# Kernel optimization log

Measured on AMD Instinct MI355X. Metric: run time of the kernel, lower is better.

## Reference

```python
import jax, jax.numpy as jnp
import numpy as np

B, L, D = 2, 2048, 1024
H = 16
HD = D // H  # 64
WINDOW = 256


def setup_inputs() -> dict:
    key = jax.random.key(0)
    k1, k2, k3 = jax.random.split(key, 3)
    s = 0.02
    return {
        "x": jax.random.normal(k1, (B, L, D), dtype=jnp.float32),
        "w_qkv": jax.random.normal(k2, (D, 3 * D), dtype=jnp.float32) * s,
        "b_qkv": jnp.zeros((3 * D,), dtype=jnp.float32),
        "w_out": jax.random.normal(k3, (D, D), dtype=jnp.float32) * s,
        "b_out": jnp.zeros((D,), dtype=jnp.float32),
    }


def _window_mask(seq_len, window_size, dtype):
    # row i allows cols in [i - w//2, i + w//2] inclusive (symmetric band)
    half = window_size // 2
    i = jnp.arange(seq_len)[:, None]
    j = jnp.arange(seq_len)[None, :]
    allowed = jnp.abs(i - j) <= half
    return jnp.where(allowed, jnp.zeros((), dtype), jnp.asarray(-jnp.inf, dtype))


def reference(x, w_qkv, b_qkv, w_out, b_out):
    b, l, d = x.shape
    qkv = x @ w_qkv + b_qkv                        # [B, L, 3D]
    qkv = qkv.reshape(b, l, 3, H, HD)
    q = jnp.transpose(qkv[:, :, 0], (0, 2, 1, 3))   # [B, H, L, HD]
    k = jnp.transpose(qkv[:, :, 1], (0, 2, 1, 3))
    v = jnp.transpose(qkv[:, :, 2], (0, 2, 1, 3))
    scale = 1.0 / np.sqrt(HD)
    scores = jnp.einsum("bhqd,bhkd->bhqk", q, k) * scale
    scores = scores + _window_mask(l, WINDOW, scores.dtype)[None, None]
    attn = jax.nn.softmax(scores, axis=-1)          # dropout: eval mode (p applied only in training)
    out = jnp.einsum("bhqk,bhkd->bhqd", attn, v)    # [B, H, L, HD]
    out = jnp.transpose(out, (0, 2, 1, 3)).reshape(b, l, d)
    return out @ w_out + b_out
```

## Files before the change

kernel.cpp:

```cpp
#include <hip/hip_runtime.h>
#include <math.h>

#define B_    2
#define L_    2048
#define D_    1024
#define H_    16
#define HD_   64
#define HALF_ 128
#define TQ    32
#define PST   296

typedef __attribute__((ext_vector_type(8))) short short8;
typedef __attribute__((ext_vector_type(4))) float f32x4;

__device__ __forceinline__ unsigned short f2bf(float x) {
  unsigned int u = __float_as_uint(x);
  u = (u + 0x7fffu + ((u >> 16) & 1u)) >> 16;
  return (unsigned short)u;
}

__device__ __forceinline__ void async_cp16(const unsigned short* g, unsigned short* l) {
  __builtin_amdgcn_global_load_lds(
      (const __attribute__((address_space(1))) unsigned int*)g,
      (__attribute__((address_space(3))) unsigned int*)l, 16, 0, 0);
}

__device__ __forceinline__ void tr_round32(const float* __restrict__ in,
                                           unsigned short* __restrict__ hi,
                                           int N, int K, int n0, int k0,
                                           float (*t)[33], int tid) {
  {
    const int kl = tid >> 3, nl = (tid & 7) * 4;
    const float4 v = *(const float4*)&in[(size_t)(k0 + kl) * N + n0 + nl];
    t[kl][nl + 0] = v.x; t[kl][nl + 1] = v.y;
    t[kl][nl + 2] = v.z; t[kl][nl + 3] = v.w;
  }
  __syncthreads();
  {
    const int no = tid >> 3, ko = (tid & 7) * 4;
    ushort4 h;
    h.x = f2bf(t[ko + 0][no]);
    h.y = f2bf(t[ko + 1][no]);
    h.z = f2bf(t[ko + 2][no]);
    h.w = f2bf(t[ko + 3][no]);
    *(ushort4*)&hi[(size_t)(n0 + no) * K + k0 + ko] = h;
  }
}

__global__ __launch_bounds__(256) void prep(const float* __restrict__ x,
                                            unsigned short* __restrict__ x_hi,
                                            const float* __restrict__ w_qkv,
                                            unsigned short* __restrict__ wqkvT,
                                            const float* __restrict__ w_out,
                                            unsigned short* __restrict__ woutT) {
  __shared__ float t[32][33];
  const int bx = blockIdx.x, tid = threadIdx.x;
  if (bx < 4096) {
    const int i = (bx * 256 + tid) * 4;
    const float4 a = *(const float4*)&x[i];
    ushort4 h;
    h.x = f2bf(a.x); h.y = f2bf(a.y); h.z = f2bf(a.z); h.w = f2bf(a.w);
    *(ushort4*)&x_hi[i] = h;
  } else if (bx < 7168) {
    const int tb = bx - 4096;
    tr_round32(w_qkv, wqkvT, 3 * D_, D_, (tb % 96) * 32, (tb / 96) * 32, t, tid);
  } else {
    const int tb = bx - 7168;
    tr_round32(w_out, woutT, D_, D_, (tb % 32) * 32, (tb / 32) * 32, t, tid);
  }
}

__global__ __launch_bounds__(256, 3) void gemm_qkv(
    const unsigned short* __restrict__ Ah,
    const unsigned short* __restrict__ Bh,
    const float* __restrict__ bias,
    unsigned short* __restrict__ q_hi,
    unsigned short* __restrict__ kT,
    unsigned short* __restrict__ vTile,
    int N, int K) {
  __shared__ char smraw[33792];
  const int tid  = threadIdx.x;
  const int wave = tid >> 6, lane = tid & 63;

  const int lin = blockIdx.y * gridDim.x + blockIdx.x;
  const int swz = (lin & 7) * 96 + (lin >> 3);
  const int n0 = (swz % 24) * 128, m0 = (swz / 24) * 128;

  const int wm = (wave >> 1) * 64, wn = (wave & 1) * 64;
  const int quad = lane >> 4, ln16 = lane & 15;

  const bool isA = wave < 2;
  const unsigned short* src = isA ? Ah : Bh;
  const int baserow = isA ? m0 : n0;
  const int instbase = (wave & 1) * 8;
  const int dbase = (isA ? 0 : 16384) + instbase * 1024;
  size_t goff[8];
#pragma unroll
  for (int i = 0; i < 8; ++i) {
    const int r = (instbase + i) * 8 + (lane >> 3);
    const int c = (lane & 7) ^ (r & 7);
    goff[i] = (size_t)(baserow + r) * K + c * 8;
  }

  int offA[4], offB[4];
#pragma unroll
  for (int t = 0; t < 4; ++t) {
    const int r = wm + t * 16 + ln16;
    offA[t] = r * 128 + ((quad ^ (r & 7)) * 16);
    const int rn = wn + t * 16 + ln16;
    offB[t] = 16384 + rn * 128 + ((quad ^ (rn & 7)) * 16);
  }

  f32x4 acc[4][4] = {};
  const char* smb = (const char*)smraw;

  for (int k0 = 0; k0 < K; k0 += 64) {
#pragma unroll
    for (int i = 0; i < 8; ++i)
      async_cp16(src + goff[i] + k0,
                 (unsigned short*)(smraw + dbase + i * 1024));
    __syncthreads();

    {
      short8 ah[4], bh[4];
#pragma unroll
      for (int t = 0; t < 4; ++t) {
        ah[t] = *(const short8*)(smb + offA[t]);
        bh[t] = *(const short8*)(smb + offB[t]);
      }
#pragma unroll
      for (int t = 0; t < 4; ++t)
#pragma unroll
        for (int u = 0; u < 4; ++u)
          acc[t][u] = __builtin_amdgcn_mfma_f32_16x16x32_bf16(bh[u], ah[t], acc[t][u], 0, 0, 0);
    }
    {
      short8 ah[4], bh[4];
#pragma unroll
      for (int t = 0; t < 4; ++t) {
        ah[t] = *(const short8*)(smb + (offA[t] ^ 64));
        bh[t] = *(const short8*)(smb + (offB[t] ^ 64));
      }
#pragma unroll
      for (int t = 0; t < 4; ++t)
#pragma unroll
        for (int u = 0; u < 4; ++u)
          acc[t][u] = __builtin_amdgcn_mfma_f32_16x16x32_bf16(bh[u], ah[t], acc[t][u], 0, 0, 0);
    }
    __syncthreads();
  }

  const int slot = n0 >> 10;
  const int nbase = n0 & 1023;

  if (slot == 0) {
#pragma unroll
    for (int t = 0; t < 4; ++t) {
      const int m = m0 + wm + t * 16 + ln16;
#pragma unroll
      for (int u = 0; u < 4; ++u) {
        const int nl = wn + u * 16 + quad * 4;
        const float4 bq = *(const float4*)&bias[n0 + nl];
        ushort4 h;
        h.x = f2bf(acc[t][u][0] + bq.x);
        h.y = f2bf(acc[t][u][1] + bq.y);
        h.z = f2bf(acc[t][u][2] + bq.z);
        h.w = f2bf(acc[t][u][3] + bq.w);
        *(ushort4*)&q_hi[(size_t)m * 1024 + nbase + nl] = h;
      }
    }
  } else if (slot == 1) {
#pragma unroll
    for (int t = 0; t < 4; ++t) {
      const int tok = m0 + wm + t * 16 + ln16;
      const int bb = tok >> 11, j = tok & 2047;
#pragma unroll
      for (int u = 0; u < 4; ++u) {
        const int nl = wn + u * 16 + quad * 4;
        const float4 bq = *(const float4*)&bias[n0 + nl];
        const int hd = nbase + nl;
        const int hh_ = hd >> 6, dg = (hd & 63) >> 3, di = hd & 7;
        ushort4 h;
        h.x = f2bf(acc[t][u][0] + bq.x);
        h.y = f2bf(acc[t][u][1] + bq.y);
        h.z = f2bf(acc[t][u][2] + bq.z);
        h.w = f2bf(acc[t][u][3] + bq.w);
        const size_t o =
            ((((size_t)bb * 16 + hh_) * 8 + dg) * 2048 + j) * 8 + di;
        *(ushort4*)&kT[o] = h;
      }
    }
  } else {
    unsigned short* lt = (unsigned short*)smraw;
#pragma unroll
    for (int t = 0; t < 4; ++t) {
      const int ml = wm + t * 16 + ln16;
#pragma unroll
      for (int u = 0; u < 4; ++u) {
        const int nl = wn + u * 16 + quad * 4;
        const float4 bq = *(const float4*)&bias[n0 + nl];
        ushort4 h;
        h.x = f2bf(acc[t][u][0] + bq.x);
        h.y = f2bf(acc[t][u][1] + bq.y);
        h.z = f2bf(acc[t][u][2] + bq.z);
        h.w = f2bf(acc[t][u][3] + bq.w);
        *(ushort4*)&lt[ml * 132 + nl] = h;
      }
    }
    __syncthreads();
    const int jg0 = (m0 & 2047) >> 3;
    const int bb = m0 >> 11;
#pragma unroll
    for (int it = 0; it < 8; ++it) {
      const int chunk = it * 256 + tid;
      const int hd = chunk & 127, tokg = chunk >> 7;
      short8 hh;
#pragma unroll
      for (int s = 0; s < 8; ++s)
        hh[s] = (short)lt[(tokg * 8 + s) * 132 + hd];
      const size_t o =
          (((size_t)bb * 256 + jg0 + tokg) * 1024 + nbase + hd) * 8;
      *(short8*)&vTile[o] = hh;
    }
  }
}

__global__ __launch_bounds__(256, 2) void gemm_out(
    const unsigned short* __restrict__ Ah,
    const unsigned short* __restrict__ Bh,
    const float* __restrict__ bias,
    float* __restrict__ C,
    int N, int K) {
  __shared__ char smraw[24576];
  const int tid  = threadIdx.x;
  const int wave = tid >> 6, lane = tid & 63;

  const int lin = blockIdx.y * gridDim.x + blockIdx.x;
  const int swz = (lin & 7) * 64 + (lin >> 3);
  const int n0 = (swz % 16) * 64, m0 = (swz / 16) * 128;

  const int quad = lane >> 4, ln16 = lane & 15;
  const int wm = wave * 32;

  const unsigned short* sptr[6];
  int dstoff[6];
#pragma unroll
  for (int s = 0; s < 6; ++s) {
    const int g = wave * 6 + s;
    const bool isA = g < 16;
    const unsigned short* base = isA ? Ah : Bh;
    const int r0 = isA ? g * 8 : (g - 16) * 8;
    const int r = r0 + (lane >> 3);
    const int c = (lane & 7) ^ (r & 7);
    sptr[s] = base + (size_t)((isA ? m0 : n0) + r) * K + c * 8;
    dstoff[s] = isA ? g * 1024 : 16384 + (g - 16) * 1024;
  }

  int offA[2], offB[4];
#pragma unroll
  for (int t = 0; t < 2; ++t) {
    const int r = wm + t * 16 + ln16;
    offA[t] = r * 128 + ((quad ^ (r & 7)) * 16);
  }
#pragma unroll
  for (int u = 0; u < 4; ++u) {
    const int rn = u * 16 + ln16;
    offB[u] = 16384 + rn * 128 + ((quad ^ (rn & 7)) * 16);
  }

  f32x4 acc[2][4] = {};
  const char* smb = (const char*)smraw;

  for (int k0 = 0; k0 < K; k0 += 64) {
#pragma unroll
    for (int s = 0; s < 6; ++s)
      async_cp16(sptr[s] + k0, (unsigned short*)(smraw + dstoff[s]));
    __syncthreads();

    {
      short8 ah[2], bh[4];
#pragma unroll
      for (int t = 0; t < 2; ++t) ah[t] = *(const short8*)(smb + offA[t]);
#pragma unroll
      for (int u = 0; u < 4; ++u) bh[u] = *(const short8*)(smb + offB[u]);
#pragma unroll
      for (int t = 0; t < 2; ++t)
#pragma unroll
        for (int u = 0; u < 4; ++u)
          acc[t][u] = __builtin_amdgcn_mfma_f32_16x16x32_bf16(bh[u], ah[t], acc[t][u], 0, 0, 0);
    }
    {
      short8 ah[2], bh[4];
#pragma unroll
      for (int t = 0; t < 2; ++t) ah[t] = *(const short8*)(smb + (offA[t] ^ 64));
#pragma unroll
      for (int u = 0; u < 4; ++u) bh[u] = *(const short8*)(smb + (offB[u] ^ 64));
#pragma unroll
      for (int t = 0; t < 2; ++t)
#pragma unroll
        for (int u = 0; u < 4; ++u)
          acc[t][u] = __builtin_amdgcn_mfma_f32_16x16x32_bf16(bh[u], ah[t], acc[t][u], 0, 0, 0);
    }
    __syncthreads();
  }

#pragma unroll
  for (int t = 0; t < 2; ++t) {
    const int m = m0 + wm + t * 16 + ln16;
#pragma unroll
    for (int u = 0; u < 4; ++u) {
      const int n = n0 + u * 16 + quad * 4;
      const float4 bq = *(const float4*)&bias[n];
      float4 o;
      o.x = acc[t][u][0] + bq.x;
      o.y = acc[t][u][1] + bq.y;
      o.z = acc[t][u][2] + bq.z;
      o.w = acc[t][u][3] + bq.w;
      *(float4*)&C[(size_t)m * N + n] = o;
    }
  }
}

__global__ __launch_bounds__(256, 4) void attn_mfma(
    const unsigned short* __restrict__ q_hi,
    const unsigned short* __restrict__ kT,
    const unsigned short* __restrict__ vTile,
    unsigned short* __restrict__ attn_h) {
  __shared__ unsigned short P[TQ * PST];
  __shared__ float redS[2][32];

  const int b   = blockIdx.z;
  const int h   = blockIdx.y;
  const int i0  = blockIdx.x * TQ;
  const int tid = threadIdx.x;
  const int wave = tid >> 6, lane = tid & 63;
  const int quad = lane >> 4, ln16 = lane & 15;
  const int mt = wave >> 1, np = wave & 1;
  const int jlo = i0 - HALF_;
  const int rbase = mt * 16 + quad * 4;

  float s[4] = {0.f, 0.f, 0.f, 0.f};
  {
    const size_t qbase =
        (size_t)(b * L_ + i0 + mt * 16 + ln16) * 1024 + h * 64 + quad * 8;
    const short8 qh0 = *(const short8*)&q_hi[qbase];
    const short8 qh1 = *(const short8*)&q_hi[qbase + 32];

    const size_t kb0 = (((size_t)b * 16 + h) * 8 + quad) * 2048 * 8;
    const size_t kb1 = (((size_t)b * 16 + h) * 8 + quad + 4) * 2048 * 8;

#pragma unroll
    for (int c = 0; c < 9; ++c) {
      const int nt   = np + 2 * c;
      const int jabs = jlo + nt * 16 + ln16;
      const int jcl  = min(max(jabs, 0), L_ - 1);
      const short8 kh0 = *(const short8*)&kT[kb0 + (size_t)jcl * 8];
      const short8 kh1 = *(const short8*)&kT[kb1 + (size_t)jcl * 8];

      f32x4 a = {};
      a = __builtin_amdgcn_mfma_f32_16x16x32_bf16(qh0, kh0, a, 0, 0, 0);
      a = __builtin_amdgcn_mfma_f32_16x16x32_bf16(qh1, kh1, a, 0, 0, 0);

      const int colj = nt * 16 + ln16;
#pragma unroll
      for (int e = 0; e < 4; ++e) {
        const int iabs = i0 + rbase + e;
        const bool ok = (jabs >= 0) && (jabs < L_) && (abs(iabs - jabs) <= HALF_);
        const float ev = ok ? __expf(a[e] * 0.125f) : 0.f;
        s[e] += ev;
        P[(rbase + e) * PST + colj] = f2bf(ev);
      }
    }
  }
#pragma unroll
  for (int e = 0; e < 4; ++e) {
    s[e] += __shfl_xor(s[e], 1);
    s[e] += __shfl_xor(s[e], 2);
    s[e] += __shfl_xor(s[e], 4);
    s[e] += __shfl_xor(s[e], 8);
  }
  if (ln16 == 0) {
#pragma unroll
    for (int e = 0; e < 4; ++e) redS[np][rbase + e] = s[e];
  }
  __syncthreads();
  float rinv[4];
#pragma unroll
  for (int e = 0; e < 4; ++e) rinv[e] = 1.f / (s[e] + redS[np ^ 1][rbase + e]);

  f32x4 o[2] = {};
  {
    const int dp = np;
    const char* pb = (const char*)P;
#pragma unroll
    for (int c = 0; c < 9; ++c) {
      const short8 pf =
          *(const short8*)(pb + (mt * 16 + ln16) * (PST * 2) + c * 64 + quad * 16);
      int j0 = jlo + c * 32 + quad * 8;
      j0 = min(max(j0, 0), L_ - 8);
      const size_t jgbase = ((size_t)b * 256 + (j0 >> 3)) * 1024;
#pragma unroll
      for (int t = 0; t < 2; ++t) {
        const size_t vb = (jgbase + (h * 64 + dp * 32 + t * 16 + ln16)) * 8;
        const short8 vh = *(const short8*)&vTile[vb];
        o[t] = __builtin_amdgcn_mfma_f32_16x16x32_bf16(pf, vh, o[t], 0, 0, 0);
      }
    }
  }

  __syncthreads();
  float* ob = (float*)P;
  {
    const int dp = np;
#pragma unroll
    for (int t = 0; t < 2; ++t)
#pragma unroll
      for (int e = 0; e < 4; ++e)
        ob[(rbase + e) * 68 + dp * 32 + t * 16 + ln16] = o[t][e] * rinv[e];
  }
  __syncthreads();
  {
    const int rr = tid >> 3, ck = tid & 7;
    const float* rp = ob + rr * 68 + ck * 8;
    const float4 f0 = *(const float4*)&rp[0];
    const float4 f1 = *(const float4*)&rp[4];
    short8 hh;
    hh[0] = (short)f2bf(f0.x); hh[1] = (short)f2bf(f0.y);
    hh[2] = (short)f2bf(f0.z); hh[3] = (short)f2bf(f0.w);
    hh[4] = (short)f2bf(f1.x); hh[5] = (short)f2bf(f1.y);
    hh[6] = (short)f2bf(f1.z); hh[7] = (short)f2bf(f1.w);
    const size_t oo = ((size_t)(b * L_ + i0 + rr)) * 1024 + h * 64 + ck * 8;
    *(short8*)&attn_h[oo] = hh;
  }
}

extern "C" void kernel_launch(void* const* d_in, const int* in_sizes, int n_in,
                              void* d_out, int out_size, void* d_ws, size_t ws_size,
                              hipStream_t stream) {
  const float* x     = (const float*)d_in[0];
  const float* w_qkv = (const float*)d_in[1];
  const float* b_qkv = (const float*)d_in[2];
  const float* w_out = (const float*)d_in[3];
  const float* b_out = (const float*)d_in[4];
  float* out = (float*)d_out;

  const int M = B_ * L_;

  char* ws = (char*)d_ws;
  unsigned short* x_hi    = (unsigned short*)(ws + 0);
  unsigned short* wqkvT   = (unsigned short*)(ws + 16777216);
  unsigned short* woutT   = (unsigned short*)(ws + 23068672);
  unsigned short* q_hi    = (unsigned short*)(ws + 25165824);
  unsigned short* kT      = (unsigned short*)(ws + 33554432);
  unsigned short* vTile   = (unsigned short*)(ws + 41943040);
  unsigned short* attn_hi = (unsigned short*)(ws + 0);

  prep<<<8192, 256, 0, stream>>>(x, x_hi, w_qkv, wqkvT, w_out, woutT);
  {
    dim3 g(3072 / 128, M / 128);
    gemm_qkv<<<g, 256, 0, stream>>>(x_hi, wqkvT, b_qkv, q_hi, kT, vTile,
                                    3072, D_);
  }
  {
    dim3 g(L_ / TQ, H_, B_);
    attn_mfma<<<g, 256, 0, stream>>>(q_hi, kT, vTile, attn_hi);
  }
  {
    dim3 g(D_ / 64, M / 128);
    gemm_out<<<g, 256, 0, stream>>>(attn_hi, woutT, b_out, out, D_, D_);
  }
}
```

Before: 158.8 us.

## Fuse QK and PV in registers, computing transposed scores to skip LDS staging

The attention kernel now computes K·Q^T so each lane holds scores for one query row. It repacks the exponentiated bf16 probabilities into the PV MFMA operand with cross-lane shuffles instead of writing the P tile to shared memory. Each wave handles 16 query rows across all 64 head dims, and a block covers 64 queries over 10 key chunks instead of 9, which adds some masked MFMA work. The change removes the P staging buffer, the cross-wave row-sum reduction and one barrier, at the cost of more shuffles, more registers and a lost occupancy hint.

```diff
diff --git a/kernel.cpp b/kernel.cpp
--- a/kernel.cpp
+++ b/kernel.cpp
@@ -7,8 +7,6 @@
 #define H_    16
 #define HD_   64
 #define HALF_ 128
-#define TQ    32
-#define PST   296
 
 typedef __attribute__((ext_vector_type(8))) short short8;
 typedef __attribute__((ext_vector_type(4))) float f32x4;
@@ -321,107 +319,123 @@
   }
 }
 
-__global__ __launch_bounds__(256, 4) void attn_mfma(
+__global__ __launch_bounds__(256) void attn_mfma(
     const unsigned short* __restrict__ q_hi,
     const unsigned short* __restrict__ kT,
     const unsigned short* __restrict__ vTile,
     unsigned short* __restrict__ attn_h) {
-  __shared__ unsigned short P[TQ * PST];
-  __shared__ float redS[2][32];
+  __shared__ float ob[64 * 68];
 
   const int b   = blockIdx.z;
   const int h   = blockIdx.y;
-  const int i0  = blockIdx.x * TQ;
+  const int i0  = blockIdx.x * 64;
   const int tid = threadIdx.x;
-  const int wave = tid >> 6, lane = tid & 63;
+  const int mt  = tid >> 6, lane = tid & 63;
   const int quad = lane >> 4, ln16 = lane & 15;
-  const int mt = wave >> 1, np = wave & 1;
   const int jlo = i0 - HALF_;
-  const int rbase = mt * 16 + quad * 4;
-
-  float s[4] = {0.f, 0.f, 0.f, 0.f};
-  {
-    const size_t qbase =
-        (size_t)(b * L_ + i0 + mt * 16 + ln16) * 1024 + h * 64 + quad * 8;
-    const short8 qh0 = *(const short8*)&q_hi[qbase];
-    const short8 qh1 = *(const short8*)&q_hi[qbase + 32];
-
-    const size_t kb0 = (((size_t)b * 16 + h) * 8 + quad) * 2048 * 8;
-    const size_t kb1 = (((size_t)b * 16 + h) * 8 + quad + 4) * 2048 * 8;
-
-#pragma unroll
-    for (int c = 0; c < 9; ++c) {
-      const int nt   = np + 2 * c;
-      const int jabs = jlo + nt * 16 + ln16;
-      const int jcl  = min(max(jabs, 0), L_ - 1);
-      const short8 kh0 = *(const short8*)&kT[kb0 + (size_t)jcl * 8];
-      const short8 kh1 = *(const short8*)&kT[kb1 + (size_t)jcl * 8];
-
-      f32x4 a = {};
-      a = __builtin_amdgcn_mfma_f32_16x16x32_bf16(qh0, kh0, a, 0, 0, 0);
-      a = __builtin_amdgcn_mfma_f32_16x16x32_bf16(qh1, kh1, a, 0, 0, 0);
-
-      const int colj = nt * 16 + ln16;
+
+  const size_t qbase =
+      (size_t)(b * L_ + i0 + mt * 16 + ln16) * 1024 + h * 64 + quad * 8;
+  const short8 qh0 = *(const short8*)&q_hi[qbase];
+  const short8 qh1 = *(const short8*)&q_hi[qbase + 32];
+
+  const size_t kb0 = (((size_t)b * 16 + h) * 8 + quad) * 2048 * 8;
+  const size_t kb1 = (((size_t)b * 16 + h) * 8 + quad + 4) * 2048 * 8;
+
+  const int iabs = i0 + mt * 16 + ln16;
+
+  f32x4 o[4] = {};
+  float s = 0.f;
+
+#pragma unroll
+  for (int c = 0; c < 10; ++c) {
+    const int base = jlo + c * 32;
+
+    const int j0c = min(max(base + ln16, 0), L_ - 1);
+    const int j1c = min(max(base + 16 + ln16, 0), L_ - 1);
+    const short8 k00 = *(const short8*)&kT[kb0 + (size_t)j0c * 8];
+    const short8 k01 = *(const short8*)&kT[kb1 + (size_t)j0c * 8];
+    const short8 k10 = *(const short8*)&kT[kb0 + (size_t)j1c * 8];
+    const short8 k11 = *(const short8*)&kT[kb1 + (size_t)j1c * 8];
+
+    const int jv = min(max(base + quad * 8, 0), L_ - 8);
+    const size_t vgb = ((size_t)b * 256 + (jv >> 3)) * 1024 + h * 64;
+    short8 vh[4];
+#pragma unroll
+    for (int t = 0; t < 4; ++t)
+      vh[t] = *(const short8*)&vTile[(vgb + t * 16 + ln16) * 8];
+
+    f32x4 a0 = {}, a1 = {};
+    a0 = __builtin_amdgcn_mfma_f32_16x16x32_bf16(k00, qh0, a0, 0, 0, 0);
+    a0 = __builtin_amdgcn_mfma_f32_16x16x32_bf16(k01, qh1, a0, 0, 0, 0);
+    a1 = __builtin_amdgcn_mfma_f32_16x16x32_bf16(k10, qh0, a1, 0, 0, 0);
+    a1 = __builtin_amdgcn_mfma_f32_16x16x32_bf16(k11, qh1, a1, 0, 0, 0);
+
+    unsigned int pk00, pk01, pk10, pk11;
+    {
+      float ev[4];
 #pragma unroll
       for (int e = 0; e < 4; ++e) {
-        const int iabs = i0 + rbase + e;
+        const int jabs = base + quad * 4 + e;
         const bool ok = (jabs >= 0) && (jabs < L_) && (abs(iabs - jabs) <= HALF_);
-        const float ev = ok ? __expf(a[e] * 0.125f) : 0.f;
-        s[e] += ev;
-        P[(rbase + e) * PST + colj] = f2bf(ev);
-      }
-    }
-  }
-#pragma unroll
-  for (int e = 0; e < 4; ++e) {
-    s[e] += __shfl_xor(s[e], 1);
-    s[e] += __shfl_xor(s[e], 2);
-    s[e] += __shfl_xor(s[e], 4);
-    s[e] += __shfl_xor(s[e], 8);
-  }
-  if (ln16 == 0) {
-#pragma unroll
-    for (int e = 0; e < 4; ++e) redS[np][rbase + e] = s[e];
-  }
+        ev[e] = ok ? __expf(a0[e] * 0.125f) : 0.f;
+        s += ev[e];
+      }
+      pk00 = (unsigned)f2bf(ev[0]) | ((unsigned)f2bf(ev[1]) << 16);
+      pk01 = (unsigned)f2bf(ev[2]) | ((unsigned)f2bf(ev[3]) << 16);
+    }
+    {
+      float ev[4];
+#pragma unroll
+      for (int e = 0; e < 4; ++e) {
+        const int jabs = base + 16 + quad * 4 + e;
+        const bool ok = (jabs >= 0) && (jabs < L_) && (abs(iabs - jabs) <= HALF_);
+        ev[e] = ok ? __expf(a1[e] * 0.125f) : 0.f;
+        s += ev[e];
+      }
+      pk10 = (unsigned)f2bf(ev[0]) | ((unsigned)f2bf(ev[1]) << 16);
+      pk11 = (unsigned)f2bf(ev[2]) | ((unsigned)f2bf(ev[3]) << 16);
+    }
+
+    const int src0 = ((quad & 1) * 2) * 16 + ln16;
+    const int src1 = src0 + 16;
+    const unsigned a0w = (unsigned)__shfl((int)pk00, src0);
+    const unsigned b0w = (unsigned)__shfl((int)pk10, src0);
+    const unsigned a1w = (unsigned)__shfl((int)pk01, src0);
+    const unsigned b1w = (unsigned)__shfl((int)pk11, src0);
+    const unsigned a2w = (unsigned)__shfl((int)pk00, src1);
+    const unsigned b2w = (unsigned)__shfl((int)pk10, src1);
+    const unsigned a3w = (unsigned)__shfl((int)pk01, src1);
+    const unsigned b3w = (unsigned)__shfl((int)pk11, src1);
+    int4 wv;
+    wv.x = (int)((quad < 2) ? a0w : b0w);
+    wv.y = (int)((quad < 2) ? a1w : b1w);
+    wv.z = (int)((quad < 2) ? a2w : b2w);
+    wv.w = (int)((quad < 2) ? a3w : b3w);
+    const short8 pf = *(const short8*)&wv;
+
+#pragma unroll
+    for (int t = 0; t < 4; ++t)
+      o[t] = __builtin_amdgcn_mfma_f32_16x16x32_bf16(pf, vh[t], o[t], 0, 0, 0);
+  }
+
+  s += __shfl_xor(s, 16);
+  s += __shfl_xor(s, 32);
+  float rinv[4];
+#pragma unroll
+  for (int e = 0; e < 4; ++e)
+    rinv[e] = 1.f / __shfl(s, quad * 4 + e);
+
+#pragma unroll
+  for (int t = 0; t < 4; ++t)
+#pragma unroll
+    for (int e = 0; e < 4; ++e)
+      ob[(mt * 16 + quad * 4 + e) * 68 + t * 16 + ln16] = o[t][e] * rinv[e];
   __syncthreads();
-  float rinv[4];
-#pragma unroll
-  for (int e = 0; e < 4; ++e) rinv[e] = 1.f / (s[e] + redS[np ^ 1][rbase + e]);
-
-  f32x4 o[2] = {};
-  {
-    const int dp = np;
-    const char* pb = (const char*)P;
-#pragma unroll
-    for (int c = 0; c < 9; ++c) {
-      const short8 pf =
-          *(const short8*)(pb + (mt * 16 + ln16) * (PST * 2) + c * 64 + quad * 16);
-      int j0 = jlo + c * 32 + quad * 8;
-      j0 = min(max(j0, 0), L_ - 8);
-      const size_t jgbase = ((size_t)b * 256 + (j0 >> 3)) * 1024;
-#pragma unroll
-      for (int t = 0; t < 2; ++t) {
-        const size_t vb = (jgbase + (h * 64 + dp * 32 + t * 16 + ln16)) * 8;
-        const short8 vh = *(const short8*)&vTile[vb];
-        o[t] = __builtin_amdgcn_mfma_f32_16x16x32_bf16(pf, vh, o[t], 0, 0, 0);
-      }
-    }
-  }
-
-  __syncthreads();
-  float* ob = (float*)P;
-  {
-    const int dp = np;
-#pragma unroll
-    for (int t = 0; t < 2; ++t)
-#pragma unroll
-      for (int e = 0; e < 4; ++e)
-        ob[(rbase + e) * 68 + dp * 32 + t * 16 + ln16] = o[t][e] * rinv[e];
-  }
-  __syncthreads();
-  {
-    const int rr = tid >> 3, ck = tid & 7;
-    const float* rp = ob + rr * 68 + ck * 8;
+#pragma unroll
+  for (int pass = 0; pass < 2; ++pass) {
+    const int rr = pass * 32 + (tid >> 3), ck = tid & 7;
+    const float* rp = &ob[rr * 68 + ck * 8];
     const float4 f0 = *(const float4*)&rp[0];
     const float4 f1 = *(const float4*)&rp[4];
     short8 hh;
@@ -462,7 +476,7 @@
                                     3072, D_);
   }
   {
-    dim3 g(L_ / TQ, H_, B_);
+    dim3 g(L_ / 64, H_, B_);
     attn_mfma<<<g, 256, 0, stream>>>(q_hi, kT, vTile, attn_hi);
   }
   {
```

Result: no change. 157.4 us (-0.9%).
